# Optimization experiments

Hardware: AMD Instinct MI355X
Metric: run time of the kernel (lower is better)

## Reference

```python
import jax, jax.numpy as jnp
import numpy as np

# SLAY feature-map hyperparams (must match init_kwargs)
H, D, P, M, R = 4, 128, 16, 32, 2   # heads, head_dim, poly_dim, num_features, quad nodes
EPS = 1e-6
C = 2.0 + EPS
_nodes, _weights = np.polynomial.laguerre.laggauss(R)
QUAD_NODES = jnp.asarray(_nodes, jnp.float32) / C
QUAD_WEIGHTS = jnp.asarray(_weights, jnp.float32) / C

VOCAB, NUM_LABELS, EMBED_DIM = 100000, 32768, 512
B, S, K = 512, 64, 5


def slay_features(x, omega, anchors):
    """SLAY feature map: tensor product of anchored polynomial and PRF features.
    x: [N, EMBED_DIM] -> [N, R*H*P*M]"""
    N = x.shape[0]
    xr = x.reshape(N, H, D)
    xn = xr / jnp.clip(jnp.linalg.norm(xr, axis=-1, keepdims=True), 1e-6)  # safe_normalize
    # anchored polynomial features: [N, H, P]
    poly_feat = jnp.einsum('nhd,pd->nhp', xn, anchors) ** 2 / jnp.sqrt(float(P))
    # positive random features with Gauss-Laguerre quadrature: [R, N, H, M]
    prf_proj = jnp.einsum('nhd,rhdm->rnhm', xn, omega)
    s = QUAD_NODES.reshape(R, 1, 1, 1)
    sqrt_2s = jnp.sqrt(2.0 * jnp.clip(s, 0))
    prf_feat = jnp.exp(jnp.clip(prf_proj * sqrt_2s - s, -10.0, 10.0)) / jnp.sqrt(float(M))
    prf_feat = prf_feat * jnp.sqrt(jnp.clip(QUAD_WEIGHTS.reshape(R, 1, 1, 1), 0))
    # tensor-product fusion: [N, R, H, P, M] -> [N, R*H*P*M]
    fused = jnp.einsum('nhp,rnhm->nrhpm', poly_feat, prf_feat)
    return fused.reshape(N, -1)


def mean_embedding(indices, mask, embedding_table):
    embeds = embedding_table[indices]                       # [B, S, E]
    sum_embeds = jnp.sum(embeds * mask[:, :, None], axis=1)  # [B, E]
    sum_mask = jnp.sum(mask, axis=1, keepdims=True)
    return sum_embeds / jnp.clip(sum_mask, 1e-9)


def setup_inputs() -> dict:
    key = jax.random.key(0)
    k1, k2, k3, k4, k5, k6 = jax.random.split(key, 6)
    indices = jax.random.randint(k1, (B, S), 0, VOCAB)
    mask = jnp.ones((B, S), dtype=jnp.float32)
    labels = jax.random.randint(k2, (B, K), 0, NUM_LABELS)
    label_mask = jnp.ones((B, K), dtype=jnp.float32)
    embedding_table = jax.random.normal(k3, (VOCAB, EMBED_DIM), dtype=jnp.float32) * 0.02
    classifier_kernel = jax.random.normal(k4, (EMBED_DIM, NUM_LABELS), dtype=jnp.float32) * 0.02
    omega = jax.random.normal(k5, (R, H, D, M), dtype=jnp.float32)
    anchors = jax.random.normal(k6, (P, D), dtype=jnp.float32)
    anchors = anchors / jnp.linalg.norm(anchors, axis=-1, keepdims=True)
    return {"indices": indices, "mask": mask, "labels": labels, "label_mask": label_mask,
            "embedding_table": embedding_table, "classifier_kernel": classifier_kernel,
            "omega": omega, "anchors": anchors}


def reference(indices, mask, labels, label_mask, embedding_table, classifier_kernel, omega, anchors):
    query = mean_embedding(indices, mask, embedding_table)            # [B, E]
    phi_query = slay_features(query, omega, anchors)                  # [B, F]
    W_vecs = classifier_kernel.T                                      # [L, E]
    phi_W = slay_features(W_vecs, omega, anchors)                     # [L, F]  (dominant cost)
    Z_approx_vec = jnp.sum(phi_W, axis=0)                             # [F]
    denom = jnp.dot(phi_query, Z_approx_vec) + 1e-6                   # [B]
    log_Z = jnp.log(denom)
    safe_labels = jnp.maximum(labels, 0)
    W_pos = W_vecs[safe_labels]                                       # [B, K, E]
    phi_w_pos = slay_features(W_pos.reshape(-1, EMBED_DIM), omega, anchors).reshape(B, K, -1)
    nums = jnp.sum(phi_w_pos * phi_query[:, None, :], axis=-1) + 1e-6  # [B, K]
    log_probs = jnp.log(nums) - log_Z[:, None]
    loss_total = -jnp.sum(log_probs * label_mask)
    return loss_total / B
```

## Files before the change

kernel.cpp:

```cpp
#include <hip/hip_runtime.h>
#include <math.h>


namespace {
constexpr double Cq  = 2.0 + 1e-6;
constexpr double QN0 = 0.5857864376269049  / Cq;
constexpr double QN1 = 3.414213562373095   / Cq;
constexpr double QW0 = 0.8535533905932738  / Cq;
constexpr double QW1 = 0.14644660940672624 / Cq;

constexpr size_t OFF_POLYQ = 0;
constexpr size_t OFF_PRFQ  = 32768;
constexpr size_t OFF_Z     = OFF_PRFQ + 131072;
constexpr size_t OFF_ANCT  = OFF_Z + 4096;
constexpr size_t OFF_SLOT  = OFF_ANCT + 2048;
constexpr size_t OFF_FEAT  = OFF_SLOT + 32768;
}

__device__ __forceinline__ void accum_feat(const float* __restrict__ x, long xstride,
                                           const float* __restrict__ anct,
                                           const float* __restrict__ omega, int h,
                                           float& sumsq, float poly[16], float prf[64])
{
    for (int d = 0; d < 128; ++d) {
        float xv = x[(long)d * xstride];
        sumsq = fmaf(xv, xv, sumsq);
        const float4* a4 = (const float4*)(anct + d * 16);
#pragma unroll
        for (int j = 0; j < 4; ++j) {
            float4 a = a4[j];
            poly[4*j+0] = fmaf(xv, a.x, poly[4*j+0]);
            poly[4*j+1] = fmaf(xv, a.y, poly[4*j+1]);
            poly[4*j+2] = fmaf(xv, a.z, poly[4*j+2]);
            poly[4*j+3] = fmaf(xv, a.w, poly[4*j+3]);
        }
#pragma unroll
        for (int r = 0; r < 2; ++r) {
            const float4* w4 = (const float4*)(omega + (((r*4 + h)*128 + d) * 32));
#pragma unroll
            for (int j = 0; j < 8; ++j) {
                float4 w = w4[j];
                prf[r*32 + 4*j+0] = fmaf(xv, w.x, prf[r*32 + 4*j+0]);
                prf[r*32 + 4*j+1] = fmaf(xv, w.y, prf[r*32 + 4*j+1]);
                prf[r*32 + 4*j+2] = fmaf(xv, w.z, prf[r*32 + 4*j+2]);
                prf[r*32 + 4*j+3] = fmaf(xv, w.w, prf[r*32 + 4*j+3]);
            }
        }
    }
}

__device__ __forceinline__ void finalize_feat(float sumsq, float poly[16], float prf[64])
{
    float rn = 1.0f / fmaxf(sqrtf(sumsq), 1e-6f);
#pragma unroll
    for (int p = 0; p < 16; ++p) { float v = poly[p] * rn; poly[p] = v * v * 0.25f; }
    const float s0 = (float)QN0, s1 = (float)QN1;
    const float g0 = sqrtf(2.0f * (float)QN0), g1 = sqrtf(2.0f * (float)QN1);
    const float c0 = sqrtf((float)QW0) * 0.17677669529663687f;
    const float c1 = sqrtf((float)QW1) * 0.17677669529663687f;
#pragma unroll
    for (int m = 0; m < 32; ++m) {
        float z0 = prf[m]      * rn * g0 - s0;
        float z1 = prf[32 + m] * rn * g1 - s1;
        z0 = fminf(fmaxf(z0, -10.f), 10.f);
        z1 = fminf(fmaxf(z1, -10.f), 10.f);
        prf[m]      = expf(z0) * c0;
        prf[32 + m] = expf(z1) * c1;
    }
}

__global__ void k_setup(const float* __restrict__ anchors, const int* __restrict__ labels,
                        int* __restrict__ slot, float* __restrict__ Z,
                        float* __restrict__ out, float* __restrict__ anct)
{
    int t = threadIdx.x;
    for (int i = t; i < 32768; i += 1024) slot[i] = -1;
    for (int i = t; i < 4096; i += 1024) Z[i] = 0.f;
    if (t == 0) out[0] = 0.f;
    for (int i = t; i < 2048; i += 1024) {
        int p = i & 15, d = i >> 4;
        anct[i] = anchors[p * 128 + d];
    }
    __syncthreads();
    for (int i = t; i < 2560; i += 1024) slot[max(labels[i], 0)] = i;
}

__global__ void __launch_bounds__(256) k_embed_feat(const int* __restrict__ idx,
        const float* __restrict__ mask, const float* __restrict__ emb,
        const float* __restrict__ anct, const float* __restrict__ omega,
        float* __restrict__ polyq, float* __restrict__ prfq)
{
    __shared__ float xs[512];
    __shared__ float rnS[4];
    int b = blockIdx.x, t = threadIdx.x;

    float2 acc = make_float2(0.f, 0.f);
    float msum = 0.f;
#pragma unroll 8
    for (int s = 0; s < 64; ++s) {
        float mv = mask[b * 64 + s];
        const float2* row = (const float2*)(emb + (size_t)idx[b * 64 + s] * 512);
        float2 v = row[t];
        acc.x = fmaf(mv, v.x, acc.x);
        acc.y = fmaf(mv, v.y, acc.y);
        msum += mv;
    }
    float inv = 1.0f / fmaxf(msum, 1e-9f);
    xs[2 * t]     = acc.x * inv;
    xs[2 * t + 1] = acc.y * inv;
    __syncthreads();

    int w = t >> 6, lane = t & 63;
    {
        float v0 = xs[w * 128 + lane], v1 = xs[w * 128 + 64 + lane];
        float ss = fmaf(v0, v0, v1 * v1);
#pragma unroll
        for (int o = 1; o < 64; o <<= 1) ss += __shfl_xor(ss, o, 64);
        if (lane == 0) rnS[w] = 1.0f / fmaxf(sqrtf(ss), 1e-6f);
    }
    __syncthreads();

    const float s_[2] = {(float)QN0, (float)QN1};
    const float g_[2] = {sqrtf(2.0f * (float)QN0), sqrtf(2.0f * (float)QN1)};
    const float c_[2] = {sqrtf((float)QW0) * 0.17677669529663687f,
                         sqrtf((float)QW1) * 0.17677669529663687f};

    for (int tau = t; tau < 320; tau += 256) {
        int h = tau / 80, j = tau - h * 80;
        const float* xh = xs + h * 128;
        float a = 0.f;
        if (j < 16) {
            for (int d = 0; d < 128; ++d) a = fmaf(xh[d], anct[d * 16 + j], a);
            float v = a * rnS[h];
            polyq[(b * 4 + h) * 16 + j] = v * v * 0.25f;
        } else {
            int rj = j - 16, r = rj >> 5, m = rj & 31;
            const float* om = omega + ((size_t)(r * 4 + h) * 128) * 32 + m;
            for (int d = 0; d < 128; ++d) a = fmaf(xh[d], om[d * 32], a);
            float z = a * rnS[h] * g_[r] - s_[r];
            z = fminf(fmaxf(z, -10.f), 10.f);
            prfq[((b * 2 + r) * 4 + h) * 32 + m] = expf(z) * c_[r];
        }
    }
}

__global__ void __launch_bounds__(256) k_labels(const float* __restrict__ ck,
                                                const float* __restrict__ anct,
                                                const float* __restrict__ omega,
                                                const int* __restrict__ slot,
                                                float* __restrict__ feat,
                                                float* __restrict__ Z)
{
    __shared__ float buf[11264];
    float* polyS = buf;
    float* prfS  = buf + 2560;
    float* Zp    = buf + 2560;

    int t = threadIdx.x, w = t >> 6, lane = t & 63;
    int h = blockIdx.x & 3;
    int l = (blockIdx.x >> 2) * 256 + t;

    float sumsq = 0.f, poly[16] = {}, prf[64] = {};
    accum_feat(ck + (size_t)h * 128 * 32768 + l, 32768, anct, omega, h, sumsq, poly, prf);
    finalize_feat(sumsq, poly, prf);

    int s = slot[l];
    if (s >= 0) {
        float4* dst = (float4*)(feat + ((size_t)s * 4 + h) * 80);
#pragma unroll
        for (int j = 0; j < 4; ++j)
            dst[j] = make_float4(poly[4*j], poly[4*j+1], poly[4*j+2], poly[4*j+3]);
#pragma unroll
        for (int j = 0; j < 16; ++j)
            dst[4 + j] = make_float4(prf[4*j], prf[4*j+1], prf[4*j+2], prf[4*j+3]);
    }

    int r = lane >> 5, p4 = (lane >> 3) & 3, m4 = lane & 7;
    float zacc[4][4] = {};

#pragma unroll
    for (int bi = 0; bi < 2; ++bi) {
        if ((t >> 7) == bi) {
            int tl = t & 127;
#pragma unroll
            for (int p = 0; p < 16; ++p) polyS[tl * 20 + p] = poly[p];
            float4* dst = (float4*)(prfS + tl * 68);
#pragma unroll
            for (int j = 0; j < 16; ++j)
                dst[j] = make_float4(prf[4*j], prf[4*j+1], prf[4*j+2], prf[4*j+3]);
        }
        __syncthreads();
        int q0 = w * 32;
        for (int q = 0; q < 32; ++q) {
            int row = q0 + q;
            float4 pv = *(const float4*)(polyS + row * 20 + p4 * 4);
            float4 fv = *(const float4*)(prfS + row * 68 + r * 32 + m4 * 4);
            zacc[0][0] = fmaf(pv.x, fv.x, zacc[0][0]);
            zacc[0][1] = fmaf(pv.x, fv.y, zacc[0][1]);
            zacc[0][2] = fmaf(pv.x, fv.z, zacc[0][2]);
            zacc[0][3] = fmaf(pv.x, fv.w, zacc[0][3]);
            zacc[1][0] = fmaf(pv.y, fv.x, zacc[1][0]);
            zacc[1][1] = fmaf(pv.y, fv.y, zacc[1][1]);
            zacc[1][2] = fmaf(pv.y, fv.z, zacc[1][2]);
            zacc[1][3] = fmaf(pv.y, fv.w, zacc[1][3]);
            zacc[2][0] = fmaf(pv.z, fv.x, zacc[2][0]);
            zacc[2][1] = fmaf(pv.z, fv.y, zacc[2][1]);
            zacc[2][2] = fmaf(pv.z, fv.z, zacc[2][2]);
            zacc[2][3] = fmaf(pv.z, fv.w, zacc[2][3]);
            zacc[3][0] = fmaf(pv.w, fv.x, zacc[3][0]);
            zacc[3][1] = fmaf(pv.w, fv.y, zacc[3][1]);
            zacc[3][2] = fmaf(pv.w, fv.z, zacc[3][2]);
            zacc[3][3] = fmaf(pv.w, fv.w, zacc[3][3]);
        }
        __syncthreads();
    }

#pragma unroll
    for (int i = 0; i < 4; ++i) {
        float* zp = Zp + w * 1024 + (r * 16 + p4 * 4 + i) * 32 + m4 * 4;
        *(float4*)zp = make_float4(zacc[i][0], zacc[i][1], zacc[i][2], zacc[i][3]);
    }
    __syncthreads();

    int f = t * 4;
    float4 a0 = *(const float4*)(Zp + f);
    float4 a1 = *(const float4*)(Zp + 1024 + f);
    float4 a2 = *(const float4*)(Zp + 2048 + f);
    float4 a3 = *(const float4*)(Zp + 3072 + f);
    float sx = a0.x + a1.x + a2.x + a3.x;
    float sy = a0.y + a1.y + a2.y + a3.y;
    float sz = a0.z + a1.z + a2.z + a3.z;
    float sw = a0.w + a1.w + a2.w + a3.w;
    float* zdst = Z + (f >> 9) * 2048 + h * 512 + (f & 511);
    atomicAdd(zdst + 0, sx);
    atomicAdd(zdst + 1, sy);
    atomicAdd(zdst + 2, sz);
    atomicAdd(zdst + 3, sw);
}

__global__ void k_final(const float* __restrict__ polyq, const float* __restrict__ prfq,
                        const float* __restrict__ Z, const int* __restrict__ labels,
                        const float* __restrict__ lmask, const int* __restrict__ slot,
                        const float* __restrict__ feat, float* __restrict__ out)
{
    int t = threadIdx.x, lane = t & 63;
    int b = blockIdx.x * 4 + (t >> 6);

    float acc = 0.f;
    for (int i = 0; i < 64; ++i) {
        int f = i * 64 + lane;
        int m = f & 31, p = (f >> 5) & 15, hh = (f >> 9) & 3, r = f >> 11;
        float phi = polyq[(b * 4 + hh) * 16 + p] * prfq[((b * 2 + r) * 4 + hh) * 32 + m];
        acc = fmaf(phi, Z[f], acc);
    }
#pragma unroll
    for (int o = 1; o < 64; o <<= 1) acc += __shfl_xor(acc, o, 64);
    float logZb = logf(acc + 1e-6f);

    if (lane < 20) {
        int k = lane >> 2, h = lane & 3;
        int l = max(labels[b * 5 + k], 0);
        int s = slot[l];
        const float4* f4 = (const float4*)(feat + ((size_t)s * 4 + h) * 80);
        const float* pq = polyq + (b * 4 + h) * 16;
        const float* q0 = prfq + ((b * 2 + 0) * 4 + h) * 32;
        const float* q1 = prfq + ((b * 2 + 1) * 4 + h) * 32;

        float pd = 0.f;
#pragma unroll
        for (int j = 0; j < 4; ++j) {
            float4 fp = f4[j];
            pd = fmaf(fp.x, pq[4*j+0], pd);
            pd = fmaf(fp.y, pq[4*j+1], pd);
            pd = fmaf(fp.z, pq[4*j+2], pd);
            pd = fmaf(fp.w, pq[4*j+3], pd);
        }
        float f0 = 0.f, f1 = 0.f;
#pragma unroll
        for (int j = 0; j < 8; ++j) {
            float4 fv = f4[4 + j];
            f0 = fmaf(fv.x, q0[4*j+0], f0);
            f0 = fmaf(fv.y, q0[4*j+1], f0);
            f0 = fmaf(fv.z, q0[4*j+2], f0);
            f0 = fmaf(fv.w, q0[4*j+3], f0);
            float4 fw = f4[12 + j];
            f1 = fmaf(fw.x, q1[4*j+0], f1);
            f1 = fmaf(fw.y, q1[4*j+1], f1);
            f1 = fmaf(fw.z, q1[4*j+2], f1);
            f1 = fmaf(fw.w, q1[4*j+3], f1);
        }
        float c = pd * (f0 + f1);
        c += __shfl_xor(c, 1, 64);
        c += __shfl_xor(c, 2, 64);
        if (h == 0) {
            float val = (logf(c + 1e-6f) - logZb) * lmask[b * 5 + k];
            atomicAdd(out, val * (-1.0f / 512.0f));
        }
    }
}

extern "C" void kernel_launch(void* const* d_in, const int* in_sizes, int n_in,
                              void* d_out, int out_size, void* d_ws, size_t ws_size,
                              hipStream_t stream)
{
    const int*   indices = (const int*)  d_in[0];
    const float* mask    = (const float*)d_in[1];
    const int*   labels  = (const int*)  d_in[2];
    const float* lmask   = (const float*)d_in[3];
    const float* emb     = (const float*)d_in[4];
    const float* ck      = (const float*)d_in[5];
    const float* omega   = (const float*)d_in[6];
    const float* anchors = (const float*)d_in[7];
    float* ws  = (float*)d_ws;
    float* out = (float*)d_out;
    int*   slot = (int*)(ws + OFF_SLOT);
    float* feat = ws + OFF_FEAT;

    k_setup<<<1, 1024, 0, stream>>>(anchors, labels, slot, ws + OFF_Z, out, ws + OFF_ANCT);
    k_embed_feat<<<512, 256, 0, stream>>>(indices, mask, emb, ws + OFF_ANCT, omega,
                                          ws + OFF_POLYQ, ws + OFF_PRFQ);
    k_labels<<<512, 256, 0, stream>>>(ck, ws + OFF_ANCT, omega, slot, feat, ws + OFF_Z);
    k_final<<<128, 256, 0, stream>>>(ws + OFF_POLYQ, ws + OFF_PRFQ, ws + OFF_Z,
                                     labels, lmask, slot, feat, out);
}
```

Baseline: 460.6 us.

## Split label feature projection across waves with packed weights and partial-Z reduction

Rebuilds the label feature kernel so each block handles 64 labels for one head, with three waves each computing 27 of the 80 packed projection outputs from a pre-packed anchor/omega matrix. This replaces the single thread per label that held 80 accumulators. Finalization and the Z outer-product run through shared memory, and per-block partial Z results are written to a workspace and summed by a new reduction kernel instead of global atomics per block. Setup is split into a multi-block kernel and a separate slot-scatter kernel. The goal is to cut register pressure and raise occupancy and parallelism, in exchange for two extra launches and extra workspace traffic.

```diff
diff --git a/kernel.cpp b/kernel.cpp
--- a/kernel.cpp
+++ b/kernel.cpp
@@ -15,74 +15,40 @@
 constexpr size_t OFF_ANCT  = OFF_Z + 4096;
 constexpr size_t OFF_SLOT  = OFF_ANCT + 2048;
 constexpr size_t OFF_FEAT  = OFF_SLOT + 32768;
-}
-
-__device__ __forceinline__ void accum_feat(const float* __restrict__ x, long xstride,
-                                           const float* __restrict__ anct,
-                                           const float* __restrict__ omega, int h,
-                                           float& sumsq, float poly[16], float prf[64])
-{
-    for (int d = 0; d < 128; ++d) {
-        float xv = x[(long)d * xstride];
-        sumsq = fmaf(xv, xv, sumsq);
-        const float4* a4 = (const float4*)(anct + d * 16);
-#pragma unroll
-        for (int j = 0; j < 4; ++j) {
-            float4 a = a4[j];
-            poly[4*j+0] = fmaf(xv, a.x, poly[4*j+0]);
-            poly[4*j+1] = fmaf(xv, a.y, poly[4*j+1]);
-            poly[4*j+2] = fmaf(xv, a.z, poly[4*j+2]);
-            poly[4*j+3] = fmaf(xv, a.w, poly[4*j+3]);
-        }
-#pragma unroll
-        for (int r = 0; r < 2; ++r) {
-            const float4* w4 = (const float4*)(omega + (((r*4 + h)*128 + d) * 32));
-#pragma unroll
-            for (int j = 0; j < 8; ++j) {
-                float4 w = w4[j];
-                prf[r*32 + 4*j+0] = fmaf(xv, w.x, prf[r*32 + 4*j+0]);
-                prf[r*32 + 4*j+1] = fmaf(xv, w.y, prf[r*32 + 4*j+1]);
-                prf[r*32 + 4*j+2] = fmaf(xv, w.z, prf[r*32 + 4*j+2]);
-                prf[r*32 + 4*j+3] = fmaf(xv, w.w, prf[r*32 + 4*j+3]);
-            }
-        }
-    }
-}
-
-__device__ __forceinline__ void finalize_feat(float sumsq, float poly[16], float prf[64])
-{
-    float rn = 1.0f / fmaxf(sqrtf(sumsq), 1e-6f);
-#pragma unroll
-    for (int p = 0; p < 16; ++p) { float v = poly[p] * rn; poly[p] = v * v * 0.25f; }
-    const float s0 = (float)QN0, s1 = (float)QN1;
-    const float g0 = sqrtf(2.0f * (float)QN0), g1 = sqrtf(2.0f * (float)QN1);
-    const float c0 = sqrtf((float)QW0) * 0.17677669529663687f;
-    const float c1 = sqrtf((float)QW1) * 0.17677669529663687f;
-#pragma unroll
-    for (int m = 0; m < 32; ++m) {
-        float z0 = prf[m]      * rn * g0 - s0;
-        float z1 = prf[32 + m] * rn * g1 - s1;
-        z0 = fminf(fmaxf(z0, -10.f), 10.f);
-        z1 = fminf(fmaxf(z1, -10.f), 10.f);
-        prf[m]      = expf(z0) * c0;
-        prf[32 + m] = expf(z1) * c1;
-    }
-}
-
-__global__ void k_setup(const float* __restrict__ anchors, const int* __restrict__ labels,
-                        int* __restrict__ slot, float* __restrict__ Z,
-                        float* __restrict__ out, float* __restrict__ anct)
-{
-    int t = threadIdx.x;
-    for (int i = t; i < 32768; i += 1024) slot[i] = -1;
-    for (int i = t; i < 4096; i += 1024) Z[i] = 0.f;
+constexpr size_t OFF_WPACK = OFF_FEAT + 819200;
+constexpr size_t OFF_ZPART = OFF_WPACK + 43008;
+}
+
+__global__ void k_setup_a(const float* __restrict__ anchors,
+                          const float* __restrict__ omega,
+                          int* __restrict__ slot, float* __restrict__ Z,
+                          float* __restrict__ out, float* __restrict__ anct,
+                          float* __restrict__ Wpack)
+{
+    int t = blockIdx.x * 256 + threadIdx.x;
+    for (int i = t; i < 32768; i += 16384) slot[i] = -1;
+    if (t < 4096) Z[t] = 0.f;
     if (t == 0) out[0] = 0.f;
-    for (int i = t; i < 2048; i += 1024) {
-        int p = i & 15, d = i >> 4;
-        anct[i] = anchors[p * 128 + d];
-    }
-    __syncthreads();
-    for (int i = t; i < 2560; i += 1024) slot[max(labels[i], 0)] = i;
+    if (t < 2048) {
+        int p = t & 15, d = t >> 4;
+        anct[t] = anchors[p * 128 + d];
+    }
+    for (int i = t; i < 4 * 128 * 84; i += 16384) {
+        int o = i % 84, hd = i / 84, d = hd & 127, h = hd >> 7;
+        float v = 0.f;
+        if (o < 16) v = anchors[o * 128 + d];
+        else if (o < 80) {
+            int r = (o - 16) >> 5, m = (o - 16) & 31;
+            v = omega[(((r * 4 + h) * 128) + d) * 32 + m];
+        }
+        Wpack[i] = v;
+    }
+}
+
+__global__ void k_setup_b(const int* __restrict__ labels, int* __restrict__ slot)
+{
+    int i = blockIdx.x * 256 + threadIdx.x;
+    if (i < 2560) slot[max(labels[i], 0)] = i;
 }
 
 __global__ void __launch_bounds__(256) k_embed_feat(const int* __restrict__ idx,
@@ -144,98 +110,106 @@
     }
 }
 
-__global__ void __launch_bounds__(256) k_labels(const float* __restrict__ ck,
-                                                const float* __restrict__ anct,
-                                                const float* __restrict__ omega,
+__global__ void __launch_bounds__(192) k_labels(const float* __restrict__ ck,
+                                                const float* __restrict__ Wpack,
                                                 const int* __restrict__ slot,
                                                 float* __restrict__ feat,
-                                                float* __restrict__ Z)
-{
-    __shared__ float buf[11264];
-    float* polyS = buf;
-    float* prfS  = buf + 2560;
-    float* Zp    = buf + 2560;
+                                                float* __restrict__ Zpart)
+{
+    __shared__ float ex[64 * 85];
+    __shared__ int slS[64];
 
     int t = threadIdx.x, w = t >> 6, lane = t & 63;
-    int h = blockIdx.x & 3;
-    int l = (blockIdx.x >> 2) * 256 + t;
-
-    float sumsq = 0.f, poly[16] = {}, prf[64] = {};
-    accum_feat(ck + (size_t)h * 128 * 32768 + l, 32768, anct, omega, h, sumsq, poly, prf);
-    finalize_feat(sumsq, poly, prf);
-
-    int s = slot[l];
-    if (s >= 0) {
-        float4* dst = (float4*)(feat + ((size_t)s * 4 + h) * 80);
-#pragma unroll
-        for (int j = 0; j < 4; ++j)
-            dst[j] = make_float4(poly[4*j], poly[4*j+1], poly[4*j+2], poly[4*j+3]);
-#pragma unroll
-        for (int j = 0; j < 16; ++j)
-            dst[4 + j] = make_float4(prf[4*j], prf[4*j+1], prf[4*j+2], prf[4*j+3]);
-    }
-
-    int r = lane >> 5, p4 = (lane >> 3) & 3, m4 = lane & 7;
-    float zacc[4][4] = {};
-
-#pragma unroll
-    for (int bi = 0; bi < 2; ++bi) {
-        if ((t >> 7) == bi) {
-            int tl = t & 127;
-#pragma unroll
-            for (int p = 0; p < 16; ++p) polyS[tl * 20 + p] = poly[p];
-            float4* dst = (float4*)(prfS + tl * 68);
-#pragma unroll
-            for (int j = 0; j < 16; ++j)
-                dst[j] = make_float4(prf[4*j], prf[4*j+1], prf[4*j+2], prf[4*j+3]);
-        }
-        __syncthreads();
-        int q0 = w * 32;
-        for (int q = 0; q < 32; ++q) {
-            int row = q0 + q;
-            float4 pv = *(const float4*)(polyS + row * 20 + p4 * 4);
-            float4 fv = *(const float4*)(prfS + row * 68 + r * 32 + m4 * 4);
-            zacc[0][0] = fmaf(pv.x, fv.x, zacc[0][0]);
-            zacc[0][1] = fmaf(pv.x, fv.y, zacc[0][1]);
-            zacc[0][2] = fmaf(pv.x, fv.z, zacc[0][2]);
-            zacc[0][3] = fmaf(pv.x, fv.w, zacc[0][3]);
-            zacc[1][0] = fmaf(pv.y, fv.x, zacc[1][0]);
-            zacc[1][1] = fmaf(pv.y, fv.y, zacc[1][1]);
-            zacc[1][2] = fmaf(pv.y, fv.z, zacc[1][2]);
-            zacc[1][3] = fmaf(pv.y, fv.w, zacc[1][3]);
-            zacc[2][0] = fmaf(pv.z, fv.x, zacc[2][0]);
-            zacc[2][1] = fmaf(pv.z, fv.y, zacc[2][1]);
-            zacc[2][2] = fmaf(pv.z, fv.z, zacc[2][2]);
-            zacc[2][3] = fmaf(pv.z, fv.w, zacc[2][3]);
-            zacc[3][0] = fmaf(pv.w, fv.x, zacc[3][0]);
-            zacc[3][1] = fmaf(pv.w, fv.y, zacc[3][1]);
-            zacc[3][2] = fmaf(pv.w, fv.z, zacc[3][2]);
-            zacc[3][3] = fmaf(pv.w, fv.w, zacc[3][3]);
-        }
-        __syncthreads();
-    }
-
-#pragma unroll
-    for (int i = 0; i < 4; ++i) {
-        float* zp = Zp + w * 1024 + (r * 16 + p4 * 4 + i) * 32 + m4 * 4;
-        *(float4*)zp = make_float4(zacc[i][0], zacc[i][1], zacc[i][2], zacc[i][3]);
-    }
+    int bid = blockIdx.x;
+    int g = bid >> 2, h = bid & 3;
+    int l0 = g * 64;
+
+    if (t < 64) slS[t] = slot[l0 + t];
+
+    const float* xcol = ck + (size_t)h * 128 * 32768 + l0 + lane;
+    int w27 = __builtin_amdgcn_readfirstlane(w * 27);
+    const float* wrow = Wpack + (size_t)h * 128 * 84 + w27;
+
+    float acc[27] = {};
+    float sumsq = 0.f;
+    for (int d = 0; d < 128; ++d) {
+        float xv = xcol[(size_t)d * 32768];
+        sumsq = fmaf(xv, xv, sumsq);
+        const float* c = wrow + d * 84;
+#pragma unroll
+        for (int i = 0; i < 27; ++i) acc[i] = fmaf(xv, c[i], acc[i]);
+    }
+
+#pragma unroll
+    for (int i = 0; i < 27; ++i) ex[lane * 85 + w27 + i] = acc[i];
+    if (w == 2) ex[lane * 85 + 80] = sumsq;
     __syncthreads();
 
-    int f = t * 4;
-    float4 a0 = *(const float4*)(Zp + f);
-    float4 a1 = *(const float4*)(Zp + 1024 + f);
-    float4 a2 = *(const float4*)(Zp + 2048 + f);
-    float4 a3 = *(const float4*)(Zp + 3072 + f);
-    float sx = a0.x + a1.x + a2.x + a3.x;
-    float sy = a0.y + a1.y + a2.y + a3.y;
-    float sz = a0.z + a1.z + a2.z + a3.z;
-    float sw = a0.w + a1.w + a2.w + a3.w;
-    float* zdst = Z + (f >> 9) * 2048 + h * 512 + (f & 511);
-    atomicAdd(zdst + 0, sx);
-    atomicAdd(zdst + 1, sy);
-    atomicAdd(zdst + 2, sz);
-    atomicAdd(zdst + 3, sw);
+    {
+        int l = t & 63, part = t >> 6, o0 = part * 27;
+        float rn = 1.0f / fmaxf(sqrtf(ex[l * 85 + 80]), 1e-6f);
+        const float s_[2] = {(float)QN0, (float)QN1};
+        const float g_[2] = {sqrtf(2.0f * (float)QN0), sqrtf(2.0f * (float)QN1)};
+        const float c_[2] = {sqrtf((float)QW0) * 0.17677669529663687f,
+                             sqrtf((float)QW1) * 0.17677669529663687f};
+#pragma unroll
+        for (int i = 0; i < 27; ++i) {
+            int o = o0 + i;
+            if (o >= 80) break;
+            float v = ex[l * 85 + o];
+            if (o < 16) {
+                v = v * rn;
+                v = v * v * 0.25f;
+            } else {
+                int r = (o - 16) >> 5;
+                float z = v * rn * g_[r] - s_[r];
+                z = fminf(fmaxf(z, -10.f), 10.f);
+                v = expf(z) * c_[r];
+            }
+            ex[l * 85 + o] = v;
+        }
+    }
+    __syncthreads();
+
+    for (int j = 0; j < 64; ++j) {
+        int s = slS[j];
+        if (s >= 0 && t < 80)
+            feat[((size_t)s * 4 + h) * 80 + t] = ex[j * 85 + t];
+    }
+
+    if (t < 128) {
+        int r = t >> 6, p0 = ((t >> 3) & 7) * 2, m0 = (t & 7) * 4;
+        float z0[4] = {}, z1[4] = {};
+        for (int j = 0; j < 64; ++j) {
+            const float* row = ex + j * 85;
+            float pa = row[p0], pb = row[p0 + 1];
+            const float* pf = row + 16 + r * 32 + m0;
+#pragma unroll
+            for (int k = 0; k < 4; ++k) {
+                float fv = pf[k];
+                z0[k] = fmaf(pa, fv, z0[k]);
+                z1[k] = fmaf(pb, fv, z1[k]);
+            }
+        }
+        float* zp = Zpart + (size_t)bid * 1024;
+#pragma unroll
+        for (int k = 0; k < 4; ++k) {
+            zp[(r * 16 + p0) * 32 + m0 + k]     = z0[k];
+            zp[(r * 16 + p0 + 1) * 32 + m0 + k] = z1[k];
+        }
+    }
+}
+
+__global__ void k_zreduce(const float* __restrict__ Zpart, float* __restrict__ Z)
+{
+    int tid = blockIdx.x * 256 + threadIdx.x;
+    int e = tid & 1023, h = (tid >> 10) & 3, chunk = tid >> 12;
+    float sum = 0.f;
+    int g0 = chunk * 64;
+#pragma unroll 4
+    for (int g = g0; g < g0 + 64; ++g)
+        sum += Zpart[(size_t)((g << 2) | h) * 1024 + e];
+    atomicAdd(&Z[(e >> 9) * 2048 + h * 512 + (e & 511)], sum);
 }
 
 __global__ void k_final(const float* __restrict__ polyq, const float* __restrict__ prfq,
@@ -314,12 +288,15 @@
     float* ws  = (float*)d_ws;
     float* out = (float*)d_out;
     int*   slot = (int*)(ws + OFF_SLOT);
-    float* feat = ws + OFF_FEAT;
-
-    k_setup<<<1, 1024, 0, stream>>>(anchors, labels, slot, ws + OFF_Z, out, ws + OFF_ANCT);
+
+    k_setup_a<<<64, 256, 0, stream>>>(anchors, omega, slot, ws + OFF_Z, out,
+                                      ws + OFF_ANCT, ws + OFF_WPACK);
+    k_setup_b<<<10, 256, 0, stream>>>(labels, slot);
     k_embed_feat<<<512, 256, 0, stream>>>(indices, mask, emb, ws + OFF_ANCT, omega,
                                           ws + OFF_POLYQ, ws + OFF_PRFQ);
-    k_labels<<<512, 256, 0, stream>>>(ck, ws + OFF_ANCT, omega, slot, feat, ws + OFF_Z);
+    k_labels<<<2048, 192, 0, stream>>>(ck, ws + OFF_WPACK, slot,
+                                       ws + OFF_FEAT, ws + OFF_ZPART);
+    k_zreduce<<<128, 256, 0, stream>>>(ws + OFF_ZPART, ws + OFF_Z);
     k_final<<<128, 256, 0, stream>>>(ws + OFF_POLYQ, ws + OFF_PRFQ, ws + OFF_Z,
-                                     labels, lmask, slot, feat, out);
-}
+                                     labels, lmask, slot, ws + OFF_FEAT, out);
+}
```

Result: faster. 415.0 us (-9.9%).
